# Kernel tuning notes

Measured on AMD Instinct MI355X. Metric: run time of the kernel, lower is better.

## Reference

```python
import jax, jax.numpy as jnp
import numpy as np

B, M, T, N = 128, 256, 512, 512

def setup_inputs() -> dict:
    key = jax.random.key(0)
    ks = jax.random.split(key, 6)
    return {
        "hidden_state": jax.random.normal(ks[0], (B, M), jnp.float32),
        "cell_state": jax.random.normal(ks[1], (B, M), jnp.float32),
        "X": jax.random.normal(ks[2], (B, T, N), jnp.float32),
        "We1": jax.random.normal(ks[3], (2 * M, T), jnp.float32) * 0.05,
        "be1": jnp.zeros((T,), jnp.float32),
        "We2": jax.random.normal(ks[4], (T, T), jnp.float32) * 0.05,
        "be2": jnp.zeros((T,), jnp.float32),
        "v": jax.random.normal(ks[5], (T, 1), jnp.float32) * 0.05,
        "bv": jnp.zeros((1,), jnp.float32),
    }

def reference(hidden_state, cell_state, X, We1, be1, We2, be2, v, bv):
    # concat hidden + cell: [B, 2m]; Dense(T) then broadcast over n (K.repeat)
    hc = jnp.concatenate([hidden_state, cell_state], axis=-1)
    hs = (hc @ We1 + be1)[:, None, :]                 # [B, 1, T] (broadcast over n)
    # Permute X -> [B, n, T], Dense(T): contract over T
    ux = jnp.einsum('btn,tk->bnk', X, We2) + be2      # [B, n, T]
    # add + tanh + Dense(1) fused chain
    e = jnp.tanh(hs + ux) @ v + bv                    # [B, n, 1]
    # Permute -> [B, 1, n], softmax over last axis (n)
    attn = jax.nn.softmax(jnp.swapaxes(e, 1, 2), axis=-1)  # [B, 1, n]
    return attn
```

## Files before the change

kernel.cpp:

```cpp
#include <hip/hip_runtime.h>
#include <hip/hip_bf16.h>


typedef _Float16 half8 __attribute__((ext_vector_type(8)));
typedef _Float16 half4 __attribute__((ext_vector_type(4)));
typedef float floatx4 __attribute__((ext_vector_type(4)));

__device__ __forceinline__ float fast_tanh(float x) {
    float cx = fminf(15.0f, fmaxf(-15.0f, x));
    float e = __expf(2.0f * cx);
    return (e - 1.0f) * __fdividef(1.0f, e + 1.0f);
}

__global__ __launch_bounds__(256) void k_prep_a(const float* __restrict__ We2,
                                                _Float16* __restrict__ Af) {
    __shared__ float w2[32][512];
    const int ts = blockIdx.x;
    for (int idx = threadIdx.x; idx < 32 * 512; idx += 256) {
        int tl = idx >> 9, k = idx & 511;
        w2[tl][k] = We2[(ts * 32 + tl) * 512 + k];
    }
    __syncthreads();
    for (int item = threadIdx.x; item < 32 * 64; item += 256) {
        int c = item >> 6, l = item & 63;
        int k  = (c >> 2) * 64 + (c & 3) * 16 + (l & 15);
        int tl = (l >> 4) * 8;
        half8 h;
#pragma unroll
        for (int j = 0; j < 8; ++j) h[j] = (_Float16)w2[tl + j][k];
        *(half8*)&Af[(((size_t)ts * 32 + c) * 64 + l) * 8] = h;
    }
}

__global__ __launch_bounds__(256) void k_hs(const float* __restrict__ hidden,
                                            const float* __restrict__ cell,
                                            const float* __restrict__ We1,
                                            const float* __restrict__ be1,
                                            const float* __restrict__ be2,
                                            float* __restrict__ g) {
    __shared__ __align__(16) float hcl[8][512];
    __shared__ float red[4][8][64];
    const int b0 = (blockIdx.x >> 3) << 3;
    const int k0 = (blockIdx.x & 7) << 6;
    for (int idx = threadIdx.x; idx < 8 * 512; idx += 256) {
        int bi = idx >> 9, j = idx & 511;
        hcl[bi][j] = (j < 256) ? hidden[(b0 + bi) * 256 + j]
                               : cell[(b0 + bi) * 256 + j - 256];
    }
    __syncthreads();
    const int kl = threadIdx.x & 63;
    const int jc = threadIdx.x >> 6;
    const int k  = k0 + kl;
    float acc[8] = {};
    for (int j = jc * 128; j < jc * 128 + 128; j += 4) {
        float w0 = We1[(j + 0) * 512 + k];
        float w1 = We1[(j + 1) * 512 + k];
        float w2 = We1[(j + 2) * 512 + k];
        float w3 = We1[(j + 3) * 512 + k];
#pragma unroll
        for (int bi = 0; bi < 8; ++bi) {
            float4 h = *(const float4*)&hcl[bi][j];
            acc[bi] += h.x * w0 + h.y * w1 + h.z * w2 + h.w * w3;
        }
    }
#pragma unroll
    for (int bi = 0; bi < 8; ++bi) red[jc][bi][kl] = acc[bi];
    __syncthreads();
    for (int idx = threadIdx.x; idx < 512; idx += 256) {
        int bi = idx >> 6, kk = idx & 63;
        float s = red[0][bi][kk] + red[1][bi][kk] + red[2][bi][kk] + red[3][bi][kk];
        int kg = k0 + kk;
        g[(b0 + bi) * 512 + kg] = s + be1[kg] + be2[kg];
    }
}

__global__ __launch_bounds__(512, 4) void k_main(const float* __restrict__ X,
                                                 const _Float16* __restrict__ Af,
                                                 const float* __restrict__ g,
                                                 const float* __restrict__ vvec,
                                                 float* __restrict__ E) {
    __shared__ __align__(16) _Float16 Abuf[2][16384];
    __shared__ __align__(16) _Float16 Xbuf[2][2304];
    const int b    = blockIdx.x >> 3;
    const int n0   = (blockIdx.x & 7) << 6;
    const int tid  = threadIdx.x;
    const int lane = tid & 63;
    const int wv   = tid >> 6;
    const int l16  = lane & 15;
    const int lhi  = lane >> 4;

    const float* Xb = X + (size_t)b * (512 * 512);

    const int xw  = wv;
    const int xc  = lane;
    const int xwr = (xc >> 1) * 72 + (xc & 1) * 32 + ((4 * xw) ^ ((xc & 3) << 3));

    float xr0, xr1, xr2, xr3;
    half8 as0, as1, as2, as3;

    {
        const _Float16* ap = Af + (size_t)tid * 8;
        as0 = *(const half8*)(ap);
        as1 = *(const half8*)(ap + 4096);
        as2 = *(const half8*)(ap + 8192);
        as3 = *(const half8*)(ap + 12288);
        const float* xp = Xb + (size_t)(4 * xw) * 512 + n0 + xc;
        xr0 = xp[0]; xr1 = xp[512]; xr2 = xp[1024]; xr3 = xp[1536];
        _Float16* lp = &Abuf[0][tid * 8];
        *(half8*)(lp)         = as0;
        *(half8*)(lp + 4096)  = as1;
        *(half8*)(lp + 8192)  = as2;
        *(half8*)(lp + 12288) = as3;
        half4 h;
        h[0] = (_Float16)xr0; h[1] = (_Float16)xr1;
        h[2] = (_Float16)xr2; h[3] = (_Float16)xr3;
        *(half4*)&Xbuf[0][xwr] = h;
    }
    __syncthreads();

    floatx4 acc[4][4];
#pragma unroll
    for (int a = 0; a < 4; ++a)
#pragma unroll
        for (int c = 0; c < 4; ++c) acc[a][c] = (floatx4){0.f, 0.f, 0.f, 0.f};

    for (int ts = 0; ts < 16; ++ts) {
        const int cur = ts & 1;
        if (ts < 15) {
            const _Float16* ap = Af + (size_t)(ts + 1) * 16384 + (size_t)tid * 8;
            as0 = *(const half8*)(ap);
            as1 = *(const half8*)(ap + 4096);
            as2 = *(const half8*)(ap + 8192);
            as3 = *(const half8*)(ap + 12288);
            const float* xp = Xb + (size_t)((ts + 1) * 32 + 4 * xw) * 512 + n0 + xc;
            xr0 = xp[0]; xr1 = xp[512]; xr2 = xp[1024]; xr3 = xp[1536];
        }
        {
            const _Float16* Ab = &Abuf[cur][wv * 2048 + lane * 8];
            half8 af0 = *(const half8*)(Ab);
            half8 af1 = *(const half8*)(Ab + 512);
            half8 af2 = *(const half8*)(Ab + 1024);
            half8 af3 = *(const half8*)(Ab + 1536);
#pragma unroll
            for (int nf = 0; nf < 4; ++nf) {
                const int n = nf * 16 + l16;
                half8 bf = *(const half8*)&Xbuf[cur][(n >> 1) * 72 + (n & 1) * 32 +
                                                     ((lhi * 8) ^ ((l16 & 3) << 3))];
                acc[0][nf] = __builtin_amdgcn_mfma_f32_16x16x32_f16(af0, bf, acc[0][nf], 0, 0, 0);
                acc[1][nf] = __builtin_amdgcn_mfma_f32_16x16x32_f16(af1, bf, acc[1][nf], 0, 0, 0);
                acc[2][nf] = __builtin_amdgcn_mfma_f32_16x16x32_f16(af2, bf, acc[2][nf], 0, 0, 0);
                acc[3][nf] = __builtin_amdgcn_mfma_f32_16x16x32_f16(af3, bf, acc[3][nf], 0, 0, 0);
            }
        }
        if (ts < 15) {
            _Float16* lp = &Abuf[cur ^ 1][tid * 8];
            *(half8*)(lp)         = as0;
            *(half8*)(lp + 4096)  = as1;
            *(half8*)(lp + 8192)  = as2;
            *(half8*)(lp + 12288) = as3;
            half4 h;
            h[0] = (_Float16)xr0; h[1] = (_Float16)xr1;
            h[2] = (_Float16)xr2; h[3] = (_Float16)xr3;
            *(half4*)&Xbuf[cur ^ 1][xwr] = h;
        }
        __syncthreads();
    }

    const float* gb = g + b * 512;
    float s[4] = {0.f, 0.f, 0.f, 0.f};
#pragma unroll
    for (int kf = 0; kf < 4; ++kf) {
        const int kb = wv * 64 + kf * 16 + lhi * 4;
        float g0 = gb[kb + 0], g1 = gb[kb + 1], g2 = gb[kb + 2], g3 = gb[kb + 3];
        float v0 = vvec[kb + 0], v1 = vvec[kb + 1], v2 = vvec[kb + 2], v3 = vvec[kb + 3];
#pragma unroll
        for (int nf = 0; nf < 4; ++nf) {
            s[nf] += fast_tanh(acc[kf][nf][0] + g0) * v0;
            s[nf] += fast_tanh(acc[kf][nf][1] + g1) * v1;
            s[nf] += fast_tanh(acc[kf][nf][2] + g2) * v2;
            s[nf] += fast_tanh(acc[kf][nf][3] + g3) * v3;
        }
    }
#pragma unroll
    for (int nf = 0; nf < 4; ++nf) {
        s[nf] += __shfl_xor(s[nf], 16);
        s[nf] += __shfl_xor(s[nf], 32);
    }
    float* ered = (float*)&Abuf[0][0];
    if (lane < 16) {
#pragma unroll
        for (int nf = 0; nf < 4; ++nf) ered[wv * 64 + nf * 16 + l16] = s[nf];
    }
    __syncthreads();
    if (tid < 64) {
        float e = 0.f;
#pragma unroll
        for (int w = 0; w < 8; ++w) e += ered[w * 64 + tid];
        E[b * 512 + n0 + tid] = e;
    }
}

__global__ __launch_bounds__(256) void k_softmax(const float* __restrict__ E,
                                                 float* __restrict__ out) {
    __shared__ float rmax[4], rsum[4];
    const int b = blockIdx.x;
    const int tid = threadIdx.x;
    float e0 = E[b * 512 + tid];
    float e1 = E[b * 512 + 256 + tid];
    float m = fmaxf(e0, e1);
    for (int o = 32; o > 0; o >>= 1) m = fmaxf(m, __shfl_xor(m, o));
    if ((tid & 63) == 0) rmax[tid >> 6] = m;
    __syncthreads();
    m = fmaxf(fmaxf(rmax[0], rmax[1]), fmaxf(rmax[2], rmax[3]));
    float p0 = __expf(e0 - m), p1 = __expf(e1 - m);
    float ss = p0 + p1;
    for (int o = 32; o > 0; o >>= 1) ss += __shfl_xor(ss, o);
    if ((tid & 63) == 0) rsum[tid >> 6] = ss;
    __syncthreads();
    ss = rsum[0] + rsum[1] + rsum[2] + rsum[3];
    float inv = __fdividef(1.0f, ss);
    out[b * 512 + tid] = p0 * inv;
    out[b * 512 + 256 + tid] = p1 * inv;
}

extern "C" void kernel_launch(void* const* d_in, const int* in_sizes, int n_in,
                              void* d_out, int out_size, void* d_ws, size_t ws_size,
                              hipStream_t stream) {
    const float* hidden = (const float*)d_in[0];
    const float* cell   = (const float*)d_in[1];
    const float* X      = (const float*)d_in[2];
    const float* We1    = (const float*)d_in[3];
    const float* be1    = (const float*)d_in[4];
    const float* We2    = (const float*)d_in[5];
    const float* be2    = (const float*)d_in[6];
    const float* v      = (const float*)d_in[7];
    float* out = (float*)d_out;

    char* ws = (char*)d_ws;
    _Float16* Af = (_Float16*)ws;
    float* g     = (float*)(ws + 524288);
    float* E     = (float*)(ws + 524288 + 262144);

    k_prep_a<<<16, 256, 0, stream>>>(We2, Af);
    k_hs<<<128, 256, 0, stream>>>(hidden, cell, We1, be1, be2, g);
    k_main<<<1024, 512, 0, stream>>>(X, Af, g, v, E);
    k_softmax<<<128, 256, 0, stream>>>(E, out);
}
```

Before: 83.33 us.

## Stage A tiles via direct global-to-LDS loads and repack X into fragment order

Weight tiles now go straight from global memory into LDS with global_load_lds, so the A prefetch no longer passes through registers or needs explicit LDS stores. The prep kernel's A layout is simplified so each wave's k-range is contiguous. X staging moves to 256 threads, each loading 8 rows and writing one half8 directly in MFMA B-fragment order, which replaces the padded, swizzled buffer and its address math. This aims to cut register pressure, VALU work and LDS bank conflicts. The trade-off is fewer threads issuing the strided X loads, plus reliance on the compiler placing the right waits for the asynchronous LDS loads; an extra barrier was also added before the reduction scratch reuse.

```diff
diff --git a/kernel.cpp b/kernel.cpp
--- a/kernel.cpp
+++ b/kernel.cpp
@@ -3,8 +3,11 @@
 
 
 typedef _Float16 half8 __attribute__((ext_vector_type(8)));
-typedef _Float16 half4 __attribute__((ext_vector_type(4)));
 typedef float floatx4 __attribute__((ext_vector_type(4)));
+
+#define GLOAD_LDS16(gp, lp) __builtin_amdgcn_global_load_lds(                  \
+    (const __attribute__((address_space(1))) void*)(const void*)(gp),          \
+    (__attribute__((address_space(3))) void*)(void*)(lp), 16, 0, 0)
 
 __device__ __forceinline__ float fast_tanh(float x) {
     float cx = fminf(15.0f, fmaxf(-15.0f, x));
@@ -23,7 +26,7 @@
     __syncthreads();
     for (int item = threadIdx.x; item < 32 * 64; item += 256) {
         int c = item >> 6, l = item & 63;
-        int k  = (c >> 2) * 64 + (c & 3) * 16 + (l & 15);
+        int k  = c * 16 + (l & 15);
         int tl = (l >> 4) * 8;
         half8 h;
 #pragma unroll
@@ -79,8 +82,8 @@
                                                  const float* __restrict__ g,
                                                  const float* __restrict__ vvec,
                                                  float* __restrict__ E) {
-    __shared__ __align__(16) _Float16 Abuf[2][16384];
-    __shared__ __align__(16) _Float16 Xbuf[2][2304];
+    __shared__ __align__(16) _Float16 Ab[2][16384];
+    __shared__ __align__(16) _Float16 Xb[2][2048];
     const int b    = blockIdx.x >> 3;
     const int n0   = (blockIdx.x & 7) << 6;
     const int tid  = threadIdx.x;
@@ -89,32 +92,26 @@
     const int l16  = lane & 15;
     const int lhi  = lane >> 4;
 
-    const float* Xb = X + (size_t)b * (512 * 512);
-
-    const int xw  = wv;
-    const int xc  = lane;
-    const int xwr = (xc >> 1) * 72 + (xc & 1) * 32 + ((4 * xw) ^ ((xc & 3) << 3));
-
-    float xr0, xr1, xr2, xr3;
-    half8 as0, as1, as2, as3;
+    const float* Xg = X + (size_t)b * (512 * 512) + n0;
+    const int  xn    = tid & 63;
+    const int  xo    = (tid >> 6) & 3;
+    const bool xact  = (tid < 256);
+    const int  xslot = ((xn >> 4) * 64 + xo * 16 + (xn & 15)) * 8;
+    const _Float16* AgW = Af + (size_t)wv * 2048 + (size_t)lane * 8;
 
     {
-        const _Float16* ap = Af + (size_t)tid * 8;
-        as0 = *(const half8*)(ap);
-        as1 = *(const half8*)(ap + 4096);
-        as2 = *(const half8*)(ap + 8192);
-        as3 = *(const half8*)(ap + 12288);
-        const float* xp = Xb + (size_t)(4 * xw) * 512 + n0 + xc;
-        xr0 = xp[0]; xr1 = xp[512]; xr2 = xp[1024]; xr3 = xp[1536];
-        _Float16* lp = &Abuf[0][tid * 8];
-        *(half8*)(lp)         = as0;
-        *(half8*)(lp + 4096)  = as1;
-        *(half8*)(lp + 8192)  = as2;
-        *(half8*)(lp + 12288) = as3;
-        half4 h;
-        h[0] = (_Float16)xr0; h[1] = (_Float16)xr1;
-        h[2] = (_Float16)xr2; h[3] = (_Float16)xr3;
-        *(half4*)&Xbuf[0][xwr] = h;
+#pragma unroll
+        for (int i = 0; i < 4; ++i)
+            GLOAD_LDS16(AgW + i * 512, &Ab[0][wv * 2048 + i * 512 + lane * 8]);
+        if (xact) {
+            float f[8];
+#pragma unroll
+            for (int j = 0; j < 8; ++j) f[j] = Xg[(size_t)(xo * 8 + j) * 512 + xn];
+            half8 h;
+#pragma unroll
+            for (int j = 0; j < 8; ++j) h[j] = (_Float16)f[j];
+            *(half8*)&Xb[0][xslot] = h;
+        }
     }
     __syncthreads();
 
@@ -124,44 +121,40 @@
 #pragma unroll
         for (int c = 0; c < 4; ++c) acc[a][c] = (floatx4){0.f, 0.f, 0.f, 0.f};
 
+    float xf[8];
     for (int ts = 0; ts < 16; ++ts) {
         const int cur = ts & 1;
+        const int nxt = cur ^ 1;
         if (ts < 15) {
-            const _Float16* ap = Af + (size_t)(ts + 1) * 16384 + (size_t)tid * 8;
-            as0 = *(const half8*)(ap);
-            as1 = *(const half8*)(ap + 4096);
-            as2 = *(const half8*)(ap + 8192);
-            as3 = *(const half8*)(ap + 12288);
-            const float* xp = Xb + (size_t)((ts + 1) * 32 + 4 * xw) * 512 + n0 + xc;
-            xr0 = xp[0]; xr1 = xp[512]; xr2 = xp[1024]; xr3 = xp[1536];
+#pragma unroll
+            for (int i = 0; i < 4; ++i)
+                GLOAD_LDS16(AgW + (size_t)(ts + 1) * 16384 + i * 512,
+                            &Ab[nxt][wv * 2048 + i * 512 + lane * 8]);
+            if (xact) {
+#pragma unroll
+                for (int j = 0; j < 8; ++j)
+                    xf[j] = Xg[(size_t)((ts + 1) * 32 + xo * 8 + j) * 512 + xn];
+            }
         }
         {
-            const _Float16* Ab = &Abuf[cur][wv * 2048 + lane * 8];
-            half8 af0 = *(const half8*)(Ab);
-            half8 af1 = *(const half8*)(Ab + 512);
-            half8 af2 = *(const half8*)(Ab + 1024);
-            half8 af3 = *(const half8*)(Ab + 1536);
+            half8 af0 = *(const half8*)&Ab[cur][(wv * 4 + 0) * 512 + lane * 8];
+            half8 af1 = *(const half8*)&Ab[cur][(wv * 4 + 1) * 512 + lane * 8];
+            half8 af2 = *(const half8*)&Ab[cur][(wv * 4 + 2) * 512 + lane * 8];
+            half8 af3 = *(const half8*)&Ab[cur][(wv * 4 + 3) * 512 + lane * 8];
 #pragma unroll
             for (int nf = 0; nf < 4; ++nf) {
-                const int n = nf * 16 + l16;
-                half8 bf = *(const half8*)&Xbuf[cur][(n >> 1) * 72 + (n & 1) * 32 +
-                                                     ((lhi * 8) ^ ((l16 & 3) << 3))];
+                half8 bf = *(const half8*)&Xb[cur][(nf * 64 + lane) * 8];
                 acc[0][nf] = __builtin_amdgcn_mfma_f32_16x16x32_f16(af0, bf, acc[0][nf], 0, 0, 0);
                 acc[1][nf] = __builtin_amdgcn_mfma_f32_16x16x32_f16(af1, bf, acc[1][nf], 0, 0, 0);
                 acc[2][nf] = __builtin_amdgcn_mfma_f32_16x16x32_f16(af2, bf, acc[2][nf], 0, 0, 0);
                 acc[3][nf] = __builtin_amdgcn_mfma_f32_16x16x32_f16(af3, bf, acc[3][nf], 0, 0, 0);
             }
         }
-        if (ts < 15) {
-            _Float16* lp = &Abuf[cur ^ 1][tid * 8];
-            *(half8*)(lp)         = as0;
-            *(half8*)(lp + 4096)  = as1;
-            *(half8*)(lp + 8192)  = as2;
-            *(half8*)(lp + 12288) = as3;
-            half4 h;
-            h[0] = (_Float16)xr0; h[1] = (_Float16)xr1;
-            h[2] = (_Float16)xr2; h[3] = (_Float16)xr3;
-            *(half4*)&Xbuf[cur ^ 1][xwr] = h;
+        if (ts < 15 && xact) {
+            half8 h;
+#pragma unroll
+            for (int j = 0; j < 8; ++j) h[j] = (_Float16)xf[j];
+            *(half8*)&Xb[nxt][xslot] = h;
         }
         __syncthreads();
     }
@@ -186,7 +179,8 @@
         s[nf] += __shfl_xor(s[nf], 16);
         s[nf] += __shfl_xor(s[nf], 32);
     }
-    float* ered = (float*)&Abuf[0][0];
+    __syncthreads();
+    float* ered = (float*)&Ab[0][0];
     if (lane < 16) {
 #pragma unroll
         for (int nf = 0; nf < 4; ++nf) ered[wv * 64 + nf * 16 + l16] = s[nf];
```

Result: no change. 83.01 us (-0.4%).
